# Kernel optimization log

Hardware: AMD Instinct MI355X
Metric: run time of the kernel (lower is better)

## Reference

```python
import jax, jax.numpy as jnp
import numpy as np

L, C, H, W = 16, 3, 512, 512
V_EPS = 1e-05


def setup_inputs() -> dict:
    key = jax.random.key(0)
    k1, k2, k3 = jax.random.split(key, 3)
    correct = jax.random.normal(k1, (L, C, H, W), dtype=jnp.float32)
    estimate = jax.random.normal(k2, (L, C, H, W), dtype=jnp.float32)
    mask = jax.random.uniform(k3, (L, C, H, W), dtype=jnp.float32)
    return {"correct": correct, "estimate": estimate, "mask": mask}


def reference(correct, estimate, mask):
    # Scale-invariant MSE, fully batched over (L, C) instead of Python loops.
    # v[l,c]   = sum_hw estimate^2 * mask
    # alpha    = sum_hw(correct*estimate*mask)/v  if v > 1e-5 else 0
    # err[l,c] = sum_hw mask * (correct - alpha*estimate)^2
    v = jnp.sum(estimate * estimate * mask, axis=(2, 3))              # [L, C]
    num = jnp.sum(correct * estimate * mask, axis=(2, 3))             # [L, C]
    cond = v > V_EPS
    alpha = jnp.where(cond, num / jnp.where(cond, v, 1.0), 0.0)       # [L, C]
    resid = correct - alpha[:, :, None, None] * estimate
    err = jnp.sum(mask * resid * resid, axis=(2, 3))                  # [L, C]
    masksum2 = jnp.sum(mask, axis=(2, 3))                             # [L, C]
    ssq = jnp.sum(err / masksum2, axis=1)                             # [L]
    return jnp.mean(ssq) / 3.0
```

## Files before the change

kernel.cpp:

```cpp
#include <hip/hip_runtime.h>

#define LDIM 16
#define CDIM 3
#define HW (512 * 512)
#define NCH (LDIM * CDIM)
#define BPC 40
#define TPB 256
#define V_EPS 1e-5

__global__ __launch_bounds__(TPB) void smse_partials(
    const float* __restrict__ correct,
    const float* __restrict__ estimate,
    const float* __restrict__ mask,
    float* __restrict__ partials)
{
    const int ch  = blockIdx.x / BPC;
    const int bin = blockIdx.x % BPC;

    const float4* __restrict__ c4 = (const float4*)(correct  + (size_t)ch * HW);
    const float4* __restrict__ e4 = (const float4*)(estimate + (size_t)ch * HW);
    const float4* __restrict__ m4 = (const float4*)(mask     + (size_t)ch * HW);
    const int N4 = HW / 4;

    float se2m = 0.f, scem = 0.f, sc2m = 0.f, sm = 0.f;
    for (int i = bin * TPB + threadIdx.x; i < N4; i += BPC * TPB) {
        float4 c = c4[i];
        float4 e = e4[i];
        float4 m = m4[i];
        se2m += e.x*e.x*m.x + e.y*e.y*m.y + e.z*e.z*m.z + e.w*e.w*m.w;
        scem += c.x*e.x*m.x + c.y*e.y*m.y + c.z*e.z*m.z + c.w*e.w*m.w;
        sc2m += c.x*c.x*m.x + c.y*c.y*m.y + c.z*c.z*m.z + c.w*c.w*m.w;
        sm   += m.x + m.y + m.z + m.w;
    }

    #pragma unroll
    for (int off = 32; off > 0; off >>= 1) {
        se2m += __shfl_down(se2m, off);
        scem += __shfl_down(scem, off);
        sc2m += __shfl_down(sc2m, off);
        sm   += __shfl_down(sm,   off);
    }

    __shared__ float4 red[TPB / 64];
    const int wave = threadIdx.x >> 6;
    const int lane = threadIdx.x & 63;
    if (lane == 0) red[wave] = make_float4(se2m, scem, sc2m, sm);
    __syncthreads();

    if (threadIdx.x == 0) {
        float4 s = red[0];
        #pragma unroll
        for (int w = 1; w < TPB / 64; ++w) {
            float4 r = red[w];
            s.x += r.x; s.y += r.y; s.z += r.z; s.w += r.w;
        }
        float* p = partials + ((size_t)ch * BPC + bin) * 4;
        p[0] = s.x; p[1] = s.y; p[2] = s.z; p[3] = s.w;
    }
}

__global__ __launch_bounds__(64) void smse_final(
    const float* __restrict__ partials,
    float* __restrict__ out)
{
    const int t = threadIdx.x;
    float val = 0.f;
    if (t < NCH) {
        double v = 0.0, num = 0.0, cc = 0.0, ms = 0.0;
        for (int b = 0; b < BPC; ++b) {
            const float* p = partials + ((size_t)t * BPC + b) * 4;
            v   += p[0];
            num += p[1];
            cc  += p[2];
            ms  += p[3];
        }
        double alpha = (v > V_EPS) ? (num / v) : 0.0;
        double err = cc - alpha * (2.0 * num - alpha * v);
        val = (float)(err / ms);
    }
    #pragma unroll
    for (int off = 32; off > 0; off >>= 1) val += __shfl_down(val, off);
    if (t == 0) out[0] = val / (float)NCH;
}

extern "C" void kernel_launch(void* const* d_in, const int* in_sizes, int n_in,
                              void* d_out, int out_size, void* d_ws, size_t ws_size,
                              hipStream_t stream) {
    const float* correct  = (const float*)d_in[0];
    const float* estimate = (const float*)d_in[1];
    const float* mask     = (const float*)d_in[2];
    float* out = (float*)d_out;
    float* partials = (float*)d_ws;

    smse_partials<<<NCH * BPC, TPB, 0, stream>>>(correct, estimate, mask, partials);
    smse_final<<<1, 64, 0, stream>>>(partials, out);
}
```

Measured before the change: 30.98 us.

## Fuse final reduction into partials kernel via last-block atomic counter

```diff
diff --git a/kernel.cpp b/kernel.cpp
--- a/kernel.cpp
+++ b/kernel.cpp
@@ -1,18 +1,20 @@
 #include <hip/hip_runtime.h>
 
-#define LDIM 16
-#define CDIM 3
 #define HW (512 * 512)
-#define NCH (LDIM * CDIM)
-#define BPC 40
+#define NCH 48
+#define BPC 32
 #define TPB 256
+#define GRID (NCH * BPC)
+#define ITERS (HW / 4 / (BPC * TPB))
 #define V_EPS 1e-5
 
-__global__ __launch_bounds__(TPB) void smse_partials(
+__global__ __launch_bounds__(TPB) void smse_fused(
     const float* __restrict__ correct,
     const float* __restrict__ estimate,
     const float* __restrict__ mask,
-    float* __restrict__ partials)
+    float4* __restrict__ partials,
+    unsigned int* __restrict__ counter,
+    float* __restrict__ out)
 {
     const int ch  = blockIdx.x / BPC;
     const int bin = blockIdx.x % BPC;
@@ -20,17 +22,21 @@
     const float4* __restrict__ c4 = (const float4*)(correct  + (size_t)ch * HW);
     const float4* __restrict__ e4 = (const float4*)(estimate + (size_t)ch * HW);
     const float4* __restrict__ m4 = (const float4*)(mask     + (size_t)ch * HW);
-    const int N4 = HW / 4;
+
+    const int stride = BPC * TPB;
+    int i = bin * TPB + threadIdx.x;
 
     float se2m = 0.f, scem = 0.f, sc2m = 0.f, sm = 0.f;
-    for (int i = bin * TPB + threadIdx.x; i < N4; i += BPC * TPB) {
+    #pragma unroll
+    for (int it = 0; it < ITERS; ++it, i += stride) {
         float4 c = c4[i];
         float4 e = e4[i];
         float4 m = m4[i];
-        se2m += e.x*e.x*m.x + e.y*e.y*m.y + e.z*e.z*m.z + e.w*e.w*m.w;
-        scem += c.x*e.x*m.x + c.y*e.y*m.y + c.z*e.z*m.z + c.w*e.w*m.w;
-        sc2m += c.x*c.x*m.x + c.y*c.y*m.y + c.z*c.z*m.z + c.w*c.w*m.w;
-        sm   += m.x + m.y + m.z + m.w;
+        float em;
+        em = e.x * m.x; se2m += e.x * em; scem += c.x * em; sc2m += c.x * c.x * m.x; sm += m.x;
+        em = e.y * m.y; se2m += e.y * em; scem += c.y * em; sc2m += c.y * c.y * m.y; sm += m.y;
+        em = e.z * m.z; se2m += e.z * em; scem += c.z * em; sc2m += c.z * c.z * m.z; sm += m.z;
+        em = e.w * m.w; se2m += e.w * em; scem += c.w * em; sc2m += c.w * c.w * m.w; sm += m.w;
     }
 
     #pragma unroll
@@ -42,6 +48,7 @@
     }
 
     __shared__ float4 red[TPB / 64];
+    __shared__ unsigned int isLast;
     const int wave = threadIdx.x >> 6;
     const int lane = threadIdx.x & 63;
     if (lane == 0) red[wave] = make_float4(se2m, scem, sc2m, sm);
@@ -54,33 +61,37 @@
             float4 r = red[w];
             s.x += r.x; s.y += r.y; s.z += r.z; s.w += r.w;
         }
-        float* p = partials + ((size_t)ch * BPC + bin) * 4;
-        p[0] = s.x; p[1] = s.y; p[2] = s.z; p[3] = s.w;
+        partials[(size_t)ch * BPC + bin] = s;
+        __threadfence();
+        unsigned int old = atomicAdd(counter, 1u);
+        isLast = (old == GRID - 1) ? 1u : 0u;
     }
-}
+    __syncthreads();
 
-__global__ __launch_bounds__(64) void smse_final(
-    const float* __restrict__ partials,
-    float* __restrict__ out)
-{
-    const int t = threadIdx.x;
-    float val = 0.f;
-    if (t < NCH) {
-        double v = 0.0, num = 0.0, cc = 0.0, ms = 0.0;
-        for (int b = 0; b < BPC; ++b) {
-            const float* p = partials + ((size_t)t * BPC + b) * 4;
-            v   += p[0];
-            num += p[1];
-            cc  += p[2];
-            ms  += p[3];
+    if (isLast) {
+        __threadfence();
+        const int t = threadIdx.x;
+        float val = 0.f;
+        if (t < NCH) {
+            const float* p = (const float*)(partials + (size_t)t * BPC);
+            double v = 0.0, num = 0.0, cc = 0.0, ms = 0.0;
+            for (int b = 0; b < BPC; ++b) {
+                float x0 = __hip_atomic_load(p + 4 * b + 0, __ATOMIC_RELAXED, __HIP_MEMORY_SCOPE_AGENT);
+                float x1 = __hip_atomic_load(p + 4 * b + 1, __ATOMIC_RELAXED, __HIP_MEMORY_SCOPE_AGENT);
+                float x2 = __hip_atomic_load(p + 4 * b + 2, __ATOMIC_RELAXED, __HIP_MEMORY_SCOPE_AGENT);
+                float x3 = __hip_atomic_load(p + 4 * b + 3, __ATOMIC_RELAXED, __HIP_MEMORY_SCOPE_AGENT);
+                v += x0; num += x1; cc += x2; ms += x3;
+            }
+            double alpha = (v > V_EPS) ? (num / v) : 0.0;
+            double err = cc - alpha * (2.0 * num - alpha * v);
+            val = (float)(err / ms);
         }
-        double alpha = (v > V_EPS) ? (num / v) : 0.0;
-        double err = cc - alpha * (2.0 * num - alpha * v);
-        val = (float)(err / ms);
+        if (t < 64) {
+            #pragma unroll
+            for (int off = 32; off > 0; off >>= 1) val += __shfl_down(val, off);
+            if (t == 0) out[0] = val / (float)NCH;
+        }
     }
-    #pragma unroll
-    for (int off = 32; off > 0; off >>= 1) val += __shfl_down(val, off);
-    if (t == 0) out[0] = val / (float)NCH;
 }
 
 extern "C" void kernel_launch(void* const* d_in, const int* in_sizes, int n_in,
@@ -90,8 +101,10 @@
     const float* estimate = (const float*)d_in[1];
     const float* mask     = (const float*)d_in[2];
     float* out = (float*)d_out;
-    float* partials = (float*)d_ws;
 
-    smse_partials<<<NCH * BPC, TPB, 0, stream>>>(correct, estimate, mask, partials);
-    smse_final<<<1, 64, 0, stream>>>(partials, out);
+    float4* partials = (float4*)d_ws;
+    unsigned int* counter = (unsigned int*)((char*)d_ws + GRID * sizeof(float4));
+
+    hipMemsetAsync(counter, 0, sizeof(unsigned int), stream);
+    smse_fused<<<GRID, TPB, 0, stream>>>(correct, estimate, mask, partials, counter, out);
 }
```

After: 84.44 us. +172.6%, slower.
